# Performance work log

Hardware: AMD Instinct MI355X
Metric: run time of the kernel (lower is better)

Reference implementation:

```python
import math
import jax
import jax.numpy as jnp
import numpy as np
from jax import lax

HEADS = 4
TOPK = 8


def _gelu(x):
    return jax.nn.gelu(x, approximate=False)


def _ln(x, g, b, eps=1e-5):
    m = x.mean(-1, keepdims=True)
    v = ((x - m) ** 2).mean(-1, keepdims=True)
    return (x - m) * lax.rsqrt(v + eps) * g + b


def setup_inputs() -> dict:
    key = jax.random.key(0)
    ks = jax.random.split(key, 16)
    B, T, N, C, A = 16, 16, 196, 768, 192

    def w(k, shape, s=0.02):
        return jax.random.normal(k, shape, jnp.float32) * s

    return dict(
        x=w(ks[0], (B, T, N + 1, C), 1.0),
        down_w=w(ks[1], (A, C)), down_b=jnp.zeros((A,), jnp.float32),
        ldw_w=w(ks[2], (A, 1, 3, 3), 0.1),
        lpw_w=w(ks[3], (A, A), 0.05),
        lnorm_g=jnp.ones((A,), jnp.float32), lnorm_b=jnp.zeros((A,), jnp.float32),
        tdw_w=w(ks[4], (A, 1, 3), 0.1),
        tpw_w=w(ks[5], (A, A), 0.05),
        tmlp_w1=w(ks[6], (2 * A, A), 0.05), tmlp_b1=jnp.zeros((2 * A,), jnp.float32),
        tmlp_w2=w(ks[7], (A, 2 * A), 0.05), tmlp_b2=jnp.zeros((A,), jnp.float32),
        tnorm_g=jnp.ones((A,), jnp.float32), tnorm_b=jnp.zeros((A,), jnp.float32),
        attn_in_w=w(ks[8], (3 * A, A), 0.05), attn_in_b=jnp.zeros((3 * A,), jnp.float32),
        attn_out_w=w(ks[9], (A, A), 0.05), attn_out_b=jnp.zeros((A,), jnp.float32),
        aproj_w=w(ks[10], (A, A), 0.05), aproj_b=jnp.zeros((A,), jnp.float32),
        anorm_g=jnp.ones((A,), jnp.float32), anorm_b=jnp.zeros((A,), jnp.float32),
        gate_w1=w(ks[11], (A, 2 * A), 0.05), gate_b1=jnp.zeros((A,), jnp.float32),
        gate_w2=w(ks[12], (3 * A, A), 0.05), gate_b2=jnp.zeros((3 * A,), jnp.float32),
        up_w=w(ks[13], (C, A), 0.02), up_b=jnp.zeros((C,), jnp.float32),
        cls_w=w(ks[14], (C, A), 0.02), cls_b=jnp.zeros((C,), jnp.float32),
    )


def reference(x, down_w, down_b, ldw_w, lpw_w, lnorm_g, lnorm_b, tdw_w, tpw_w,
              tmlp_w1, tmlp_b1, tmlp_w2, tmlp_b2, tnorm_g, tnorm_b,
              attn_in_w, attn_in_b, attn_out_w, attn_out_b, aproj_w, aproj_b,
              anorm_g, anorm_b, gate_w1, gate_b1, gate_w2, gate_b2,
              up_w, up_b, cls_w, cls_b):
    cls_tok = x[:, :, :1, :]
    patch = x[:, :, 1:, :]
    b, t, n, _ = patch.shape
    hw = int(math.isqrt(n))
    a = down_w.shape[0]

    # down projection: [b,t,n,C] -> [b,t,n,A]
    ph = jnp.einsum('btnc,ac->btna', patch, down_w) + down_b
    # temporal difference, delta[:,0]=0
    delta = jnp.concatenate([jnp.zeros_like(ph[:, :1]), ph[:, 1:] - ph[:, :-1]], axis=1)

    # --- local path: depthwise 3x3 -> GELU -> pointwise 1x1 -> LN ---
    loc = ph.reshape(b * t, hw, hw, a).transpose(0, 3, 1, 2)  # (bt) a h w
    loc = lax.conv_general_dilated(loc, ldw_w, (1, 1), 'SAME',
                                   feature_group_count=a,
                                   dimension_numbers=('NCHW', 'OIHW', 'NCHW'))
    loc = _gelu(loc)
    loc = jnp.einsum('bchw,dc->bdhw', loc, lpw_w)
    loc = loc.transpose(0, 2, 3, 1).reshape(b, t, n, a)
    local = _ln(loc, lnorm_g, lnorm_b)

    # --- transition path: depthwise temporal conv -> GELU -> pointwise -> MLP -> LN ---
    tr = delta.transpose(0, 2, 3, 1).reshape(b * n, a, t)  # (bn) a t
    tr = lax.conv_general_dilated(tr, tdw_w, (1,), 'SAME',
                                  feature_group_count=a,
                                  dimension_numbers=('NCH', 'OIH', 'NCH'))
    tr = _gelu(tr)
    tr = jnp.einsum('nct,dc->ndt', tr, tpw_w)
    tr = tr.reshape(b, n, a, t).transpose(0, 3, 1, 2)  # b t n a
    h1 = _gelu(jnp.einsum('btna,ha->btnh', tr, tmlp_w1) + tmlp_b1)
    tr = jnp.einsum('btnh,ah->btna', h1, tmlp_w2) + tmlp_b2
    transition = _ln(tr, tnorm_g, tnorm_b)

    # --- relation anchor path: topk gather -> temporal MHA -> scatter_add -> LN ---
    kk = min(TOPK, n)
    sal = jnp.abs(delta).mean(-1)  # b t n
    _, idx = lax.top_k(sal, kk)    # b t k
    bi = jnp.arange(b)[:, None, None]
    ti = jnp.arange(t)[None, :, None]
    anchor = (ph + delta)[bi, ti, idx]  # b t k a
    tok = anchor.transpose(0, 2, 1, 3).reshape(b * kk, t, a)  # (bk) t a
    qkv = tok @ attn_in_w.T + attn_in_b
    q, k_, v = jnp.split(qkv, 3, axis=-1)
    dh = a // HEADS

    def heads(z):
        return z.reshape(b * kk, t, HEADS, dh).transpose(0, 2, 1, 3)

    q, k_, v = heads(q), heads(k_), heads(v)
    att = jax.nn.softmax(jnp.einsum('bhqd,bhkd->bhqk', q, k_) / math.sqrt(dh), axis=-1)
    out = jnp.einsum('bhqk,bhkd->bhqd', att, v).transpose(0, 2, 1, 3).reshape(b * kk, t, a)
    out = out @ attn_out_w.T + attn_out_b
    out = out @ aproj_w.T + aproj_b
    anchor_tok = out.reshape(b, kk, t, a).transpose(0, 2, 1, 3)  # b t k a
    anchor_map = jnp.zeros_like(ph).at[bi, ti, idx].add(anchor_tok)
    anchor_map = _ln(anchor_map, anorm_g, anorm_b)

    # --- softmax-gated 3-way fusion ---
    dp = jnp.abs(delta).mean((1, 2))      # b a
    ap = anchor_tok.mean((1, 2))          # b a
    g = jnp.concatenate([dp, ap], axis=-1)
    g = _gelu(g @ gate_w1.T + gate_b1) @ gate_w2.T + gate_b2
    gw = jax.nn.softmax(g.reshape(b, 3, a), axis=1)[:, :, None, None, :]
    fused = gw[:, 0] * local + gw[:, 1] * transition + gw[:, 2] * anchor_map

    patch_out = patch + fused @ up_w.T + up_b
    cls_out = cls_tok + fused.mean(2, keepdims=True) @ cls_w.T + cls_b
    return jnp.concatenate([cls_out, patch_out], axis=2)
```

## Files before the change

### kernel.cpp

```cpp
#include <hip/hip_runtime.h>
#include <hip/hip_bf16.h>
#include <math.h>

constexpr int Bb  = 16;
constexpr int Tt  = 16;
constexpr int Nn  = 196;
constexpr int Cc  = 768;
constexpr int Aa  = 192;
constexpr int KK  = 8;
constexpr int NCAND = 16;
constexpr int BT  = Bb * Tt;
constexpr int BTN = BT * Nn;
constexpr int BKT = Bb * KK * Tt;
constexpr size_t SZ = (size_t)BTN * Aa;

typedef unsigned short ushortt;
typedef __attribute__((ext_vector_type(8))) short bf16x8;
typedef __attribute__((ext_vector_type(4))) float f32x4;
typedef __attribute__((ext_vector_type(4))) unsigned short u16x4;
typedef __attribute__((ext_vector_type(8))) unsigned short u16x8;

static __device__ __forceinline__ float gelu_f(float x) {
  return 0.5f * x * (1.0f + erff(x * 0.7071067811865476f));
}
static __device__ __forceinline__ ushortt f2bf(float f) {
  __hip_bfloat16 h = __float2bfloat16(f);
  return *reinterpret_cast<ushortt*>(&h);
}
static __device__ __forceinline__ float bf2f(ushortt u) {
  return __uint_as_float(((unsigned)u) << 16);
}

template <typename AT, typename CT, int ROWMAP, int BIAS, int EPI>
__global__ __launch_bounds__(256) void gemm_mfma(
    const AT* __restrict__ Ain, const float* __restrict__ W,
    const float* __restrict__ bias, CT* __restrict__ Cout,
    const float* __restrict__ resid, int M, int Nc, int K) {
  constexpr int PIT = 72;
  __shared__ __align__(16) unsigned char smem[(2 * 64 * PIT + 2 * 96 * PIT) * 2];
  ushortt (*As)[64 * PIT] = (ushortt(*)[64 * PIT])smem;
  ushortt (*Bs)[96 * PIT] = (ushortt(*)[96 * PIT])(smem + 2 * 64 * PIT * 2);
  const int tid = threadIdx.x;

  const int ncb = gridDim.x;
  const int nwg = ncb * gridDim.y;
  const int bid = blockIdx.y * ncb + blockIdx.x;
  const int cpx = nwg >> 3;
  const int swz = (bid & 7) * cpx + (bid >> 3);
  const int row0 = (swz / ncb) * 64;
  const int col0 = (swz % ncb) * 96;

  const int wid = tid >> 6;
  const int lane = tid & 63;
  const int wr = wid >> 1;
  const int wc = wid & 1;
  const int l15 = lane & 15;
  const int kgrp = lane >> 4;

  const int q16 = tid & 15;
  const int q8 = tid & 7;

  const int nsteps = K >> 6;

  const float* arowf[4];
  const ushortt* arowb[2];
  if constexpr (sizeof(AT) == 4) {
#pragma unroll
    for (int p = 0; p < 4; ++p) {
      int r = row0 + (tid >> 4) + 16 * p;
      if (ROWMAP) {
        int bt = r / Nn;
        int n = r - bt * Nn;
        arowf[p] = (const float*)Ain + (size_t)(bt * (Nn + 1) + 1 + n) * K;
      } else {
        arowf[p] = (const float*)Ain + (size_t)r * K;
      }
    }
  } else {
#pragma unroll
    for (int p = 0; p < 2; ++p)
      arowb[p] = (const ushortt*)Ain + (size_t)(row0 + (tid >> 3) + 32 * p) * K;
  }
  const float* browp[6];
#pragma unroll
  for (int p = 0; p < 6; ++p)
    browp[p] = W + (size_t)(col0 + (tid >> 4) + 16 * p) * K;

  f32x4 acc[2][3];
#pragma unroll
  for (int i = 0; i < 2; ++i)
#pragma unroll
    for (int j = 0; j < 3; ++j) acc[i][j] = (f32x4){0.f, 0.f, 0.f, 0.f};

  float4 apre[4], bpre[6];
  u16x8 apreb[2];

#define STAGE_LOAD(k0)                                                       \
  if constexpr (sizeof(AT) == 4) {                                           \
    _Pragma("unroll") for (int p = 0; p < 4; ++p)                            \
        apre[p] = *(const float4*)(arowf[p] + (k0) + q16 * 4);               \
  } else {                                                                   \
    _Pragma("unroll") for (int p = 0; p < 2; ++p)                            \
        apreb[p] = *(const u16x8*)(arowb[p] + (k0) + q8 * 8);                \
  }                                                                          \
  _Pragma("unroll") for (int p = 0; p < 6; ++p)                              \
      bpre[p] = *(const float4*)(browp[p] + (k0) + q16 * 4);

#define STAGE_WRITE(buf)                                                     \
  if constexpr (sizeof(AT) == 4) {                                           \
    _Pragma("unroll") for (int p = 0; p < 4; ++p) {                          \
      u16x4 b = {f2bf(apre[p].x), f2bf(apre[p].y), f2bf(apre[p].z),          \
                 f2bf(apre[p].w)};                                           \
      *(u16x4*)&As[buf][((tid >> 4) + 16 * p) * PIT + q16 * 4] = b;          \
    }                                                                        \
  } else {                                                                   \
    _Pragma("unroll") for (int p = 0; p < 2; ++p)                            \
        *(u16x8*)&As[buf][((tid >> 3) + 32 * p) * PIT + q8 * 8] = apreb[p];  \
  }                                                                          \
  _Pragma("unroll") for (int p = 0; p < 6; ++p) {                            \
    u16x4 b = {f2bf(bpre[p].x), f2bf(bpre[p].y), f2bf(bpre[p].z),            \
               f2bf(bpre[p].w)};                                             \
    *(u16x4*)&Bs[buf][((tid >> 4) + 16 * p) * PIT + q16 * 4] = b;            \
  }

  STAGE_LOAD(0);
  STAGE_WRITE(0);
  __syncthreads();

  int cur = 0;
  for (int step = 0; step < nsteps; ++step) {
    const bool pref = (step + 1 < nsteps);
    if (pref) {
      int k0 = (step + 1) << 6;
      STAGE_LOAD(k0);
    }
#pragma unroll
    for (int kk = 0; kk < 2; ++kk) {
      bf16x8 af[2], bfv[3];
#pragma unroll
      for (int fm = 0; fm < 2; ++fm)
        af[fm] = *(const bf16x8*)&As[cur][(wr * 32 + fm * 16 + l15) * PIT +
                                          kk * 32 + kgrp * 8];
#pragma unroll
      for (int fn = 0; fn < 3; ++fn)
        bfv[fn] = *(const bf16x8*)&Bs[cur][(wc * 48 + fn * 16 + l15) * PIT +
                                           kk * 32 + kgrp * 8];
#pragma unroll
      for (int fm = 0; fm < 2; ++fm)
#pragma unroll
        for (int fn = 0; fn < 3; ++fn)
          acc[fm][fn] = __builtin_amdgcn_mfma_f32_16x16x32_bf16(
              af[fm], bfv[fn], acc[fm][fn], 0, 0, 0);
    }
    if (pref) {
      STAGE_WRITE(cur ^ 1);
    }
    __syncthreads();
    cur ^= 1;
  }
#undef STAGE_LOAD
#undef STAGE_WRITE

  constexpr int EP = 100;
  float* epi = (float*)smem;
#pragma unroll
  for (int fm = 0; fm < 2; ++fm) {
    int rl = wr * 32 + fm * 16 + kgrp * 4;
#pragma unroll
    for (int fn = 0; fn < 3; ++fn) {
      int cl = wc * 48 + fn * 16 + l15;
#pragma unroll
      for (int j = 0; j < 4; ++j)
        epi[(rl + j) * EP + cl] = acc[fm][fn][j];
    }
  }
  __syncthreads();
#pragma unroll
  for (int it = 0; it < 6; ++it) {
    int f = it * 256 + tid;
    int r = f / 24, c4 = f - r * 24;
    float4 v = *(const float4*)&epi[r * EP + c4 * 4];
    int c = col0 + c4 * 4;
    if (BIAS) {
      float4 bv = *(const float4*)(bias + c);
      v.x += bv.x; v.y += bv.y; v.z += bv.z; v.w += bv.w;
    }
    if (EPI == 1) {
      v.x = gelu_f(v.x); v.y = gelu_f(v.y);
      v.z = gelu_f(v.z); v.w = gelu_f(v.w);
    }
    int R = row0 + r;
    if constexpr (EPI == 2) {
      int bt2 = R / Nn, n2 = R - bt2 * Nn;
      size_t off = (size_t)(bt2 * (Nn + 1) + 1 + n2) * Nc + c;
      float4 rv = *(const float4*)(resid + off);
      v.x += rv.x; v.y += rv.y; v.z += rv.z; v.w += rv.w;
      *(float4*)((float*)Cout + off) = v;
    } else if constexpr (sizeof(CT) == 4) {
      *(float4*)((float*)Cout + (size_t)R * Nc + c) = v;
    } else {
      u16x4 ob = {f2bf(v.x), f2bf(v.y), f2bf(v.z), f2bf(v.w)};
      *(u16x4*)((ushortt*)Cout + (size_t)R * Nc + c) = ob;
    }
  }
}

__global__ void delta_kernel(const ushortt* __restrict__ ph,
                             ushortt* __restrict__ delta,
                             float* __restrict__ dppart) {
  int bt = blockIdx.x;
  int t = bt & 15;
  int a = threadIdx.x;
  const ushortt* cur = ph + (size_t)bt * Nn * Aa + a;
  ushortt* dl = delta + (size_t)bt * Nn * Aa + a;
  float acc = 0.f;
  if (t == 0) {
    for (int n = 0; n < Nn; ++n) dl[(size_t)n * Aa] = 0;
  } else {
    const ushortt* prev = cur - (size_t)Nn * Aa;
    for (int n = 0; n < Nn; ++n) {
      float d = bf2f(cur[(size_t)n * Aa]) - bf2f(prev[(size_t)n * Aa]);
      dl[(size_t)n * Aa] = f2bf(d);
      acc += fabsf(d);
    }
  }
  dppart[bt * Aa + a] = acc;
}

__global__ void sal_kernel(const ushortt* __restrict__ delta,
                           float* __restrict__ sal) {
  int row = blockIdx.x * 4 + (threadIdx.x >> 6);
  int lane = threadIdx.x & 63;
  const ushortt* d = delta + (size_t)row * Aa;
  float s = fabsf(bf2f(d[lane])) + fabsf(bf2f(d[lane + 64])) +
            fabsf(bf2f(d[lane + 128]));
#pragma unroll
  for (int off = 32; off > 0; off >>= 1) s += __shfl_xor(s, off, 64);
  if (lane == 0) sal[row] = s * (1.0f / 192.0f);
}

__global__ void topcand_kernel(const float* __restrict__ sal,
                               int* __restrict__ cand) {
  int bt = blockIdx.x;
  int lane = threadIdx.x;
  unsigned long long key[4];
#pragma unroll
  for (int j = 0; j < 4; ++j) {
    int n = lane + 64 * j;
    if (n < Nn) {
      unsigned fb = __float_as_uint(sal[(size_t)bt * Nn + n]);
      key[j] = ((unsigned long long)fb << 32) |
               (unsigned long long)(0xFFFFFFFFu - (unsigned)n);
    } else {
      key[j] = 0ULL;
    }
  }
  for (int r = 0; r < NCAND; ++r) {
    unsigned long long m = key[0];
    if (key[1] > m) m = key[1];
    if (key[2] > m) m = key[2];
    if (key[3] > m) m = key[3];
#pragma unroll
    for (int off = 32; off > 0; off >>= 1) {
      unsigned long long o = __shfl_xor(m, off, 64);
      if (o > m) m = o;
    }
    if (lane == 0)
      cand[bt * NCAND + r] = (int)(0xFFFFFFFFu - (unsigned)(m & 0xFFFFFFFFull));
#pragma unroll
    for (int j = 0; j < 4; ++j)
      if (key[j] == m) key[j] = 0ULL;
  }
}

__global__ void transpose_w(const float* __restrict__ w,
                            float* __restrict__ wT) {
  int e = blockIdx.x * 256 + threadIdx.x;
  int c = e / Aa, a = e - c * Aa;
  wT[e] = w[(size_t)a * Cc + c];
}

__global__ __launch_bounds__(192) void refine_kernel(
    const float* __restrict__ x, const float* __restrict__ wT,
    const int* __restrict__ cand, double* __restrict__ sal64) {
  int bt = blockIdx.x;
  int grp = blockIdx.y;
  int t = bt & 15;
  int a = threadIdx.x;
  if (t == 0) {
    if (a < 8) sal64[bt * NCAND + grp * 8 + a] = 0.0;
    return;
  }
  __shared__ double sdiff[8][Cc];
  const float* xt = x + ((size_t)bt * (Nn + 1) + 1) * Cc;
  const float* xp = xt - (size_t)(Nn + 1) * Cc;
  for (int g = 0; g < 8; ++g) {
    int n = cand[bt * NCAND + grp * 8 + g];
    const float* rt = xt + (size_t)n * Cc;
    const float* rp = xp + (size_t)n * Cc;
    for (int c = a; c < Cc; c += 192)
      sdiff[g][c] = (double)rt[c] - (double)rp[c];
  }
  __syncthreads();
  double acc[8] = {};
  for (int c = 0; c < Cc; ++c) {
    double wv = (double)wT[(size_t)c * Aa + a];
#pragma unroll
    for (int g = 0; g < 8; ++g) acc[g] = fma(wv, sdiff[g][c], acc[g]);
  }
  __shared__ double part[3][8];
  int wvx = a >> 6, ln = a & 63;
#pragma unroll
  for (int g = 0; g < 8; ++g) {
    double v = fabs(acc[g]);
#pragma unroll
    for (int off = 32; off > 0; off >>= 1) v += __shfl_xor(v, off, 64);
    if (ln == 0) part[wvx][g] = v;
  }
  __syncthreads();
  if (a < 8) {
    double s = part[0][a] + part[1][a] + part[2][a];
    sal64[bt * NCAND + grp * 8 + a] = s * (1.0 / 192.0);
  }
}

__global__ void select_kernel(const double* __restrict__ sal64,
                              const int* __restrict__ cand,
                              int* __restrict__ idx) {
  int bt = blockIdx.x;
  int t = bt & 15;
  int lane = threadIdx.x;
  if (t == 0) {
    if (lane < KK) idx[bt * KK + lane] = lane;
    return;
  }
  double v = (lane < NCAND) ? sal64[bt * NCAND + lane] : -1.0;
  int n = (lane < NCAND) ? cand[bt * NCAND + lane] : 0x7FFFFFFF;
  for (int r = 0; r < KK; ++r) {
    double bv = v;
    int bn = n, bl = lane;
#pragma unroll
    for (int off = 8; off >= 1; off >>= 1) {
      double ov = __shfl_xor(bv, off, 64);
      int on = __shfl_xor(bn, off, 64);
      int ol = __shfl_xor(bl, off, 64);
      if (ov > bv || (ov == bv && on < bn)) { bv = ov; bn = on; bl = ol; }
    }
    if (lane == 0) idx[bt * KK + r] = bn;
    if (lane == bl) v = -1.0;
  }
}

__global__ void gather_kernel(const ushortt* __restrict__ ph,
                              const ushortt* __restrict__ delta,
                              const int* __restrict__ idx,
                              ushortt* __restrict__ tok) {
  int row = blockIdx.x;
  int t = row & 15;
  int bk = row >> 4;
  int b = bk >> 3, k = bk & 7;
  int a = threadIdx.x;
  int n = idx[(b * 16 + t) * KK + k];
  size_t off = ((size_t)(b * 16 + t) * Nn + n) * Aa + a;
  tok[(size_t)row * Aa + a] = f2bf(bf2f(ph[off]) + bf2f(delta[off]));
}

__global__ __launch_bounds__(256) void attn_core(
    const float* __restrict__ qkv, float* __restrict__ o) {
  constexpr int P = 580;
  __shared__ float sq[16 * P];
  __shared__ float ssc[4][16][17];
  int bk = blockIdx.x;
  int tid = threadIdx.x;
  const float* src = qkv + (size_t)bk * 16 * 576;
  for (int e = tid; e < 16 * 144; e += 256) {
    int r = e / 144, c4 = e % 144;
    float4 v = *(const float4*)(src + r * 576 + c4 * 4);
    *(float4*)(&sq[r * P + c4 * 4]) = v;
  }
  __syncthreads();
  int h = tid >> 6, lane = tid & 63;
#pragma unroll
  for (int s4 = 0; s4 < 4; ++s4) {
    int e = lane + 64 * s4;
    int i = e >> 4, j = e & 15;
    const float* q = sq + i * P + h * 48;
    const float* k2 = sq + j * P + 192 + h * 48;
    float s = 0.f;
#pragma unroll
    for (int d = 0; d < 48; ++d) s = fmaf(q[d], k2[d], s);
    ssc[h][i][j] = s * 0.14433756729740643f;
  }
  __syncthreads();
  if (lane < 16) {
    float* r = ssc[h][lane];
    float mx = r[0];
    for (int j = 1; j < 16; ++j) mx = fmaxf(mx, r[j]);
    float sum = 0.f;
    for (int j = 0; j < 16; ++j) {
      float ev = expf(r[j] - mx);
      r[j] = ev;
      sum += ev;
    }
    float inv = 1.0f / sum;
    for (int j = 0; j < 16; ++j) r[j] *= inv;
  }
  __syncthreads();
#pragma unroll
  for (int s4 = 0; s4 < 12; ++s4) {
    int e = lane + 64 * s4;
    int i = e / 48, d = e - i * 48;
    float s = 0.f;
#pragma unroll
    for (int j = 0; j < 16; ++j)
      s = fmaf(ssc[h][i][j], sq[j * P + 384 + h * 48 + d], s);
    o[((size_t)bk * 16 + i) * 192 + h * 48 + d] = s;
  }
}

__global__ void appart_kernel(const float* __restrict__ attout,
                              float* __restrict__ appart) {
  int bk = blockIdx.x;
  int a = threadIdx.x;
  float s = 0.f;
  for (int t = 0; t < Tt; ++t)
    s += attout[((size_t)bk * Tt + t) * Aa + a];
  appart[bk * Aa + a] = s;
}

__global__ void ln32_kernel(float* __restrict__ buf,
                            const float* __restrict__ g,
                            const float* __restrict__ bb) {
  size_t row = (size_t)blockIdx.x * 4 + (threadIdx.x >> 6);
  int lane = threadIdx.x & 63;
  float* p = buf + row * Aa;
  float v0 = p[lane], v1 = p[lane + 64], v2 = p[lane + 128];
  float s = v0 + v1 + v2;
#pragma unroll
  for (int off = 32; off > 0; off >>= 1) s += __shfl_xor(s, off, 64);
  float m = s * (1.0f / 192.0f);
  float d0 = v0 - m, d1 = v1 - m, d2 = v2 - m;
  float ss = d0 * d0 + d1 * d1 + d2 * d2;
#pragma unroll
  for (int off = 32; off > 0; off >>= 1) ss += __shfl_xor(ss, off, 64);
  float inv = rsqrtf(ss * (1.0f / 192.0f) + 1e-5f);
  p[lane] = d0 * inv * g[lane] + bb[lane];
  p[lane + 64] = d1 * inv * g[lane + 64] + bb[lane + 64];
  p[lane + 128] = d2 * inv * g[lane + 128] + bb[lane + 128];
}

__global__ void conv2d_kernel(const ushortt* __restrict__ ph,
                              const float* __restrict__ ldw,
                              ushortt* __restrict__ og) {
  size_t e = (size_t)blockIdx.x * 256 + threadIdx.x;
  int a = (int)(e % Aa);
  size_t r = e / Aa;
  int n = (int)(r % Nn);
  int bt = (int)(r / Nn);
  int y = n / 14, x = n % 14;
  const ushortt* base = ph + (size_t)bt * Nn * Aa + a;
  const float* w = ldw + a * 9;
  float s = 0.f;
#pragma unroll
  for (int dy = -1; dy <= 1; ++dy) {
    int yy = y + dy;
    if (yy < 0 || yy >= 14) continue;
#pragma unroll
    for (int dx = -1; dx <= 1; ++dx) {
      int xc = x + dx;
      if (xc < 0 || xc >= 14) continue;
      s = fmaf(bf2f(base[(size_t)(yy * 14 + xc) * Aa]),
               w[(dy + 1) * 3 + (dx + 1)], s);
    }
  }
  og[e] = f2bf(gelu_f(s));
}

__global__ void conv1d_kernel(const ushortt* __restrict__ delta,
                              const float* __restrict__ tdw,
                              ushortt* __restrict__ og) {
  size_t e = (size_t)blockIdx.x * 256 + threadIdx.x;
  int a = (int)(e % Aa);
  size_t r = e / Aa;
  int n = (int)(r % Nn);
  int bt = (int)(r / Nn);
  int t = bt & 15, b = bt >> 4;
  const float* w = tdw + a * 3;
  float s = 0.f;
#pragma unroll
  for (int j = 0; j < 3; ++j) {
    int tt = t + j - 1;
    if (tt >= 0 && tt < Tt)
      s = fmaf(bf2f(delta[((size_t)(b * Tt + tt) * Nn + n) * Aa + a]), w[j], s);
  }
  og[e] = f2bf(gelu_f(s));
}

__global__ void ln_kernel(ushortt* __restrict__ buf,
                          const float* __restrict__ g,
                          const float* __restrict__ bb) {
  size_t row = (size_t)blockIdx.x * 4 + (threadIdx.x >> 6);
  int lane = threadIdx.x & 63;
  ushortt* p = buf + row * Aa;
  float v0 = bf2f(p[lane]), v1 = bf2f(p[lane + 64]), v2 = bf2f(p[lane + 128]);
  float s = v0 + v1 + v2;
#pragma unroll
  for (int off = 32; off > 0; off >>= 1) s += __shfl_xor(s, off, 64);
  float m = s * (1.0f / 192.0f);
  float d0 = v0 - m, d1 = v1 - m, d2 = v2 - m;
  float ss = d0 * d0 + d1 * d1 + d2 * d2;
#pragma unroll
  for (int off = 32; off > 0; off >>= 1) ss += __shfl_xor(ss, off, 64);
  float inv = rsqrtf(ss * (1.0f / 192.0f) + 1e-5f);
  p[lane] = f2bf(d0 * inv * g[lane] + bb[lane]);
  p[lane + 64] = f2bf(d1 * inv * g[lane + 64] + bb[lane + 64]);
  p[lane + 128] = f2bf(d2 * inv * g[lane + 128] + bb[lane + 128]);
}

__global__ void scatter_pos(const int* __restrict__ idx,
                            short* __restrict__ posmap) {
  int bt = blockIdx.x;
  int k = threadIdx.x;
  if (k < KK) posmap[bt * Nn + idx[bt * KK + k]] = (short)(k + 1);
}

__global__ void gate_kernel(const float* __restrict__ dppart,
                            const float* __restrict__ appart,
                            const float* __restrict__ w1,
                            const float* __restrict__ b1,
                            const float* __restrict__ w2,
                            const float* __restrict__ b2,
                            float* __restrict__ gw) {
  int b = blockIdx.x;
  __shared__ float sg[2 * Aa];
  __shared__ float sh[Aa];
  int tid = threadIdx.x;
  {
    float d = 0.f;
    for (int t2 = 0; t2 < Tt; ++t2) d += dppart[(b * Tt + t2) * Aa + tid];
    sg[tid] = d * (1.0f / 3136.0f);
    float a = 0.f;
    for (int k2 = 0; k2 < KK; ++k2) a += appart[(b * KK + k2) * Aa + tid];
    sg[Aa + tid] = a * (1.0f / 128.0f);
  }
  __syncthreads();
  {
    const float* w = w1 + (size_t)tid * 2 * Aa;
    float s = b1[tid];
#pragma unroll 8
    for (int j = 0; j < 2 * Aa; ++j) s = fmaf(sg[j], w[j], s);
    sh[tid] = gelu_f(s);
  }
  __syncthreads();
  float v[3];
#pragma unroll
  for (int i = 0; i < 3; ++i) {
    const float* w = w2 + (size_t)(i * Aa + tid) * Aa;
    float s = b2[i * Aa + tid];
#pragma unroll 8
    for (int j = 0; j < Aa; ++j) s = fmaf(sh[j], w[j], s);
    v[i] = s;
  }
  float mx = fmaxf(v[0], fmaxf(v[1], v[2]));
  float e0 = expf(v[0] - mx), e1 = expf(v[1] - mx), e2 = expf(v[2] - mx);
  float inv = 1.0f / (e0 + e1 + e2);
  gw[(b * 3 + 0) * Aa + tid] = e0 * inv;
  gw[(b * 3 + 1) * Aa + tid] = e1 * inv;
  gw[(b * 3 + 2) * Aa + tid] = e2 * inv;
}

__global__ void fused_kernel(const ushortt* __restrict__ local,
                             const ushortt* __restrict__ trans,
                             const float* __restrict__ attln,
                             const short* __restrict__ posmap,
                             const float* __restrict__ anb,
                             const float* __restrict__ gw,
                             ushortt* __restrict__ fused,
                             float* __restrict__ fmean) {
  int bt = blockIdx.x;
  int b = bt >> 4, t = bt & 15;
  int a = threadIdx.x;
  float g0 = gw[(b * 3 + 0) * Aa + a];
  float g1 = gw[(b * 3 + 1) * Aa + a];
  float g2 = gw[(b * 3 + 2) * Aa + a];
  float ab = anb[a];
  size_t base = (size_t)bt * Nn * Aa + a;
  float acc = 0.f;
  for (int n = 0; n < Nn; ++n) {
    size_t o = base + (size_t)n * Aa;
    short pos = posmap[bt * Nn + n];
    float am = pos ? attln[(((size_t)(b * KK + pos - 1) * Tt) + t) * Aa + a]
                   : ab;
    float f = g0 * bf2f(local[o]) + g1 * bf2f(trans[o]) + g2 * am;
    fused[o] = f2bf(f);
    acc += f;
  }
  fmean[bt * Aa + a] = acc;
}

__global__ void cls_kernel(const float* __restrict__ fmean,
                           const float* __restrict__ cw,
                           const float* __restrict__ cb,
                           const float* __restrict__ x,
                           float* __restrict__ out) {
  int bt = blockIdx.x;
  __shared__ float fm[Aa];
  int tid = threadIdx.x;
  if (tid < Aa) fm[tid] = fmean[bt * Aa + tid] * (1.0f / 196.0f);
  __syncthreads();
  for (int c = tid; c < Cc; c += 256) {
    const float* w = cw + (size_t)c * Aa;
    float s = cb[c];
#pragma unroll 8
    for (int a = 0; a < Aa; ++a) s = fmaf(fm[a], w[a], s);
    size_t off = (size_t)bt * (Nn + 1) * Cc + c;
    out[off] = x[off] + s;
  }
}

extern "C" void kernel_launch(void* const* d_in, const int* in_sizes, int n_in,
                              void* d_out, int out_size, void* d_ws,
                              size_t ws_size, hipStream_t stream) {
  const float* x = (const float*)d_in[0];
  const float* down_w = (const float*)d_in[1];
  const float* down_b = (const float*)d_in[2];
  const float* ldw_w = (const float*)d_in[3];
  const float* lpw_w = (const float*)d_in[4];
  const float* lnorm_g = (const float*)d_in[5];
  const float* lnorm_b = (const float*)d_in[6];
  const float* tdw_w = (const float*)d_in[7];
  const float* tpw_w = (const float*)d_in[8];
  const float* tmlp_w1 = (const float*)d_in[9];
  const float* tmlp_b1 = (const float*)d_in[10];
  const float* tmlp_w2 = (const float*)d_in[11];
  const float* tmlp_b2 = (const float*)d_in[12];
  const float* tnorm_g = (const float*)d_in[13];
  const float* tnorm_b = (const float*)d_in[14];
  const float* attn_in_w = (const float*)d_in[15];
  const float* attn_in_b = (const float*)d_in[16];
  const float* attn_out_w = (const float*)d_in[17];
  const float* attn_out_b = (const float*)d_in[18];
  const float* aproj_w = (const float*)d_in[19];
  const float* aproj_b = (const float*)d_in[20];
  const float* anorm_g = (const float*)d_in[21];
  const float* anorm_b = (const float*)d_in[22];
  const float* gate_w1 = (const float*)d_in[23];
  const float* gate_b1 = (const float*)d_in[24];
  const float* gate_w2 = (const float*)d_in[25];
  const float* gate_b2 = (const float*)d_in[26];
  const float* up_w = (const float*)d_in[27];
  const float* up_b = (const float*)d_in[28];
  const float* cls_w = (const float*)d_in[29];
  const float* cls_b = (const float*)d_in[30];
  float* out = (float*)d_out;

  float* ws = (float*)d_ws;
  float* W0 = ws;
  float* W1 = W0 + SZ;
  float* W2 = W1 + SZ;
  float* W3 = W2 + 2 * SZ;
  float* sal = W3 + SZ;
  float* attout = sal + BTN;
  float* dppart = attout + (size_t)BKT * Aa;
  float* appart = dppart + (size_t)BT * Aa;
  float* gw = appart + (size_t)Bb * KK * Aa;
  float* fmean = gw + (size_t)Bb * 3 * Aa;
  double* sal64 = (double*)(fmean + (size_t)BT * Aa);
  int* cand = (int*)(sal64 + (size_t)BT * NCAND);
  int* idx = cand + (size_t)BT * NCAND;
  float* wT = (float*)(idx + (size_t)BT * KK);
  short* posmap = (short*)(wT + (size_t)Cc * Aa);

  ushortt* ph_b    = (ushortt*)W0;
  ushortt* trp_b   = (ushortt*)W0;
  ushortt* delta_b = (ushortt*)W1;
  ushortt* trans_b = (ushortt*)W1;
  ushortt* locg_b  = (ushortt*)W2;
  ushortt* trg_b   = (ushortt*)W2;
  ushortt* h1_b    = (ushortt*)W2;
  ushortt* fused_b = (ushortt*)W2;
  ushortt* local_b = (ushortt*)W3;

  ushortt* tok_b = (ushortt*)W2;
  float* qkvb  = W2 + (size_t)BKT * Aa / 2;
  float* obuf  = qkvb + (size_t)BKT * 3 * Aa;
  float* proj1 = obuf + (size_t)BKT * Aa;

  gemm_mfma<float, ushortt, 1, 1, 0><<<dim3(2, 784), 256, 0, stream>>>(
      x, down_w, down_b, ph_b, nullptr, BTN, Aa, Cc);
  transpose_w<<<(Cc * Aa) / 256, 256, 0, stream>>>(down_w, wT);
  delta_kernel<<<BT, Aa, 0, stream>>>(ph_b, delta_b, dppart);
  sal_kernel<<<BTN / 4, 256, 0, stream>>>(delta_b, sal);
  topcand_kernel<<<BT, 64, 0, stream>>>(sal, cand);
  refine_kernel<<<dim3(BT, 2), 192, 0, stream>>>(x, wT, cand, sal64);
  select_kernel<<<BT, 64, 0, stream>>>(sal64, cand, idx);
  gather_kernel<<<BKT, Aa, 0, stream>>>(ph_b, delta_b, idx, tok_b);
  gemm_mfma<ushortt, float, 0, 1, 0><<<dim3(6, 32), 256, 0, stream>>>(
      tok_b, attn_in_w, attn_in_b, qkvb, nullptr, BKT, 3 * Aa, Aa);
  attn_core<<<Bb * KK, 256, 0, stream>>>(qkvb, obuf);
  gemm_mfma<float, float, 0, 1, 0><<<dim3(2, 32), 256, 0, stream>>>(
      obuf, attn_out_w, attn_out_b, proj1, nullptr, BKT, Aa, Aa);
  gemm_mfma<float, float, 0, 1, 0><<<dim3(2, 32), 256, 0, stream>>>(
      proj1, aproj_w, aproj_b, attout, nullptr, BKT, Aa, Aa);
  appart_kernel<<<Bb * KK, Aa, 0, stream>>>(attout, appart);
  ln32_kernel<<<BKT / 4, 256, 0, stream>>>(attout, anorm_g, anorm_b);
  hipMemsetAsync(posmap, 0, (size_t)BT * Nn * sizeof(short), stream);
  scatter_pos<<<BT, 64, 0, stream>>>(idx, posmap);
  conv2d_kernel<<<(unsigned)(SZ / 256), 256, 0, stream>>>(ph_b, ldw_w, locg_b);
  gemm_mfma<ushortt, ushortt, 0, 0, 0><<<dim3(2, 784), 256, 0, stream>>>(
      locg_b, lpw_w, nullptr, local_b, nullptr, BTN, Aa, Aa);
  ln_kernel<<<BTN / 4, 256, 0, stream>>>(local_b, lnorm_g, lnorm_b);
  conv1d_kernel<<<(unsigned)(SZ / 256), 256, 0, stream>>>(delta_b, tdw_w, trg_b);
  gemm_mfma<ushortt, ushortt, 0, 0, 0><<<dim3(2, 784), 256, 0, stream>>>(
      trg_b, tpw_w, nullptr, trp_b, nullptr, BTN, Aa, Aa);
  gemm_mfma<ushortt, ushortt, 0, 1, 1><<<dim3(4, 784), 256, 0, stream>>>(
      trp_b, tmlp_w1, tmlp_b1, h1_b, nullptr, BTN, 2 * Aa, Aa);
  gemm_mfma<ushortt, ushortt, 0, 1, 0><<<dim3(2, 784), 256, 0, stream>>>(
      h1_b, tmlp_w2, tmlp_b2, trans_b, nullptr, BTN, Aa, 2 * Aa);
  ln_kernel<<<BTN / 4, 256, 0, stream>>>(trans_b, tnorm_g, tnorm_b);
  gate_kernel<<<Bb, Aa, 0, stream>>>(dppart, appart, gate_w1, gate_b1,
                                     gate_w2, gate_b2, gw);
  fused_kernel<<<BT, Aa, 0, stream>>>(local_b, trans_b, attout, posmap,
                                      anorm_b, gw, fused_b, fmean);
  gemm_mfma<ushortt, float, 0, 1, 2><<<dim3(8, 784), 256, 0, stream>>>(
      fused_b, up_w, up_b, out, x, BTN, Cc, Aa);
  cls_kernel<<<BT, 256, 0, stream>>>(fmean, cls_w, cls_b, x, out);
}
```

Before: 608.3 us.

## Pre-convert weights to bf16 and use direct-to-LDS loads in bf16 GEMMs

Adds a kernel that converts all GEMM weights to bf16 once per call, plus a new GEMM variant. The variant loads bf16 A and B tiles straight into LDS with global_load_lds, using an XOR-swizzled layout and double buffering. Six bf16-input GEMMs now use it, which removes the per-tile fp32-to-bf16 weight conversion and the register staging of tile data. In exchange it launches an extra conversion kernel and needs more workspace, and it assumes 16-byte alignment and M, N and K that divide evenly into tiles.

Measured after the change: 579.7 us. 1.05x faster.

```diff
diff --git a/kernel.cpp b/kernel.cpp
--- a/kernel.cpp
+++ b/kernel.cpp
@@ -29,6 +29,180 @@
 }
 static __device__ __forceinline__ float bf2f(ushortt u) {
   return __uint_as_float(((unsigned)u) << 16);
+}
+static __device__ __forceinline__ void gload16(const void* g, void* l) {
+  __builtin_amdgcn_global_load_lds(
+      (const __attribute__((address_space(1))) void*)g,
+      (__attribute__((address_space(3))) void*)l, 16, 0, 0);
+}
+
+constexpr int S_down   = Aa * Cc;
+constexpr int S_attnin = 3 * Aa * Aa;
+constexpr int S_sq     = Aa * Aa;
+constexpr int S_t      = 2 * Aa * Aa;
+constexpr int O1 = S_down;
+constexpr int O2 = O1 + S_attnin;
+constexpr int O3 = O2 + S_sq;
+constexpr int O4 = O3 + S_sq;
+constexpr int O5 = O4 + S_sq;
+constexpr int O6 = O5 + S_sq;
+constexpr int O7 = O6 + S_t;
+constexpr int O8 = O7 + S_t;
+constexpr int OTOT = O8 + S_down;
+
+__global__ void cvtw_kernel(const float* __restrict__ w0,
+                            const float* __restrict__ w1,
+                            const float* __restrict__ w2,
+                            const float* __restrict__ w3,
+                            const float* __restrict__ w4,
+                            const float* __restrict__ w5,
+                            const float* __restrict__ w6,
+                            const float* __restrict__ w7,
+                            const float* __restrict__ w8,
+                            ushortt* __restrict__ outw) {
+  int e = blockIdx.x * 256 + threadIdx.x;
+  const float* src;
+  int off;
+  if (e < O1)      { src = w0; off = 0;  }
+  else if (e < O2) { src = w1; off = O1; }
+  else if (e < O3) { src = w2; off = O2; }
+  else if (e < O4) { src = w3; off = O3; }
+  else if (e < O5) { src = w4; off = O4; }
+  else if (e < O6) { src = w5; off = O5; }
+  else if (e < O7) { src = w6; off = O6; }
+  else if (e < O8) { src = w7; off = O7; }
+  else             { src = w8; off = O8; }
+  outw[e] = f2bf(src[e - off]);
+}
+
+template <typename CT, int BIAS, int EPI>
+__global__ __launch_bounds__(256) void gemm_lds(
+    const ushortt* __restrict__ Ain, const ushortt* __restrict__ Wb,
+    const float* __restrict__ bias, CT* __restrict__ Cout,
+    const float* __restrict__ resid, int M, int Nc, int K) {
+  __shared__ __align__(16) unsigned char smem[40960];
+  ushortt (*As)[64 * 64] = (ushortt(*)[64 * 64])smem;
+  ushortt (*Bs)[96 * 64] = (ushortt(*)[96 * 64])(smem + 2 * 64 * 64 * 2);
+  const int tid = threadIdx.x;
+
+  const int ncb = gridDim.x;
+  const int nwg = ncb * gridDim.y;
+  const int bid = blockIdx.y * ncb + blockIdx.x;
+  const int cpx = nwg >> 3;
+  const int swz = (bid & 7) * cpx + (bid >> 3);
+  const int row0 = (swz / ncb) * 64;
+  const int col0 = (swz % ncb) * 96;
+
+  const int wid = tid >> 6;
+  const int lane = tid & 63;
+  const int wr = wid >> 1;
+  const int wc = wid & 1;
+  const int l15 = lane & 15;
+  const int kgrp = lane >> 4;
+
+  const int lr = lane >> 3;
+  const int lc = 8 * ((lane & 7) ^ lr);
+
+  f32x4 acc[2][3];
+#pragma unroll
+  for (int i = 0; i < 2; ++i)
+#pragma unroll
+    for (int j = 0; j < 3; ++j) acc[i][j] = (f32x4){0.f, 0.f, 0.f, 0.f};
+
+#define ISSUE(buf, k0)                                                       \
+  do {                                                                       \
+    _Pragma("unroll") for (int i = 0; i < 2; ++i) {                          \
+      int j = 2 * wid + i;                                                   \
+      const ushortt* g =                                                     \
+          Ain + (size_t)(row0 + 8 * j + lr) * K + (k0) + lc;                 \
+      gload16(g, &As[buf][j * 512]);                                         \
+    }                                                                        \
+    _Pragma("unroll") for (int i = 0; i < 3; ++i) {                          \
+      int j = 3 * wid + i;                                                   \
+      const ushortt* g =                                                     \
+          Wb + (size_t)(col0 + 8 * j + lr) * K + (k0) + lc;                  \
+      gload16(g, &Bs[buf][j * 512]);                                         \
+    }                                                                        \
+  } while (0)
+
+  ISSUE(0, 0);
+  __syncthreads();
+
+  const int nsteps = K >> 6;
+  int cur = 0;
+  for (int step = 0; step < nsteps; ++step) {
+    const bool pref = (step + 1 < nsteps);
+    if (pref) ISSUE(cur ^ 1, (step + 1) << 6);
+#pragma unroll
+    for (int kk = 0; kk < 2; ++kk) {
+      const int cb = kk * 64 + kgrp * 16;
+      bf16x8 af[2], bfv[3];
+#pragma unroll
+      for (int fm = 0; fm < 2; ++fm) {
+        int r = wr * 32 + fm * 16 + l15;
+        af[fm] = *(const bf16x8*)&As[cur][r * 64 +
+                                          ((cb ^ ((r & 7) << 4)) >> 1)];
+      }
+#pragma unroll
+      for (int fn = 0; fn < 3; ++fn) {
+        int r = wc * 48 + fn * 16 + l15;
+        bfv[fn] = *(const bf16x8*)&Bs[cur][r * 64 +
+                                           ((cb ^ ((r & 7) << 4)) >> 1)];
+      }
+#pragma unroll
+      for (int fm = 0; fm < 2; ++fm)
+#pragma unroll
+        for (int fn = 0; fn < 3; ++fn)
+          acc[fm][fn] = __builtin_amdgcn_mfma_f32_16x16x32_bf16(
+              af[fm], bfv[fn], acc[fm][fn], 0, 0, 0);
+    }
+    __syncthreads();
+    cur ^= 1;
+  }
+#undef ISSUE
+
+  constexpr int EP = 100;
+  float* epi = (float*)smem;
+#pragma unroll
+  for (int fm = 0; fm < 2; ++fm) {
+    int rl = wr * 32 + fm * 16 + kgrp * 4;
+#pragma unroll
+    for (int fn = 0; fn < 3; ++fn) {
+      int cl = wc * 48 + fn * 16 + l15;
+#pragma unroll
+      for (int j = 0; j < 4; ++j)
+        epi[(rl + j) * EP + cl] = acc[fm][fn][j];
+    }
+  }
+  __syncthreads();
+#pragma unroll
+  for (int it = 0; it < 6; ++it) {
+    int f = it * 256 + tid;
+    int r = f / 24, c4 = f - r * 24;
+    float4 v = *(const float4*)&epi[r * EP + c4 * 4];
+    int c = col0 + c4 * 4;
+    if (BIAS) {
+      float4 bv = *(const float4*)(bias + c);
+      v.x += bv.x; v.y += bv.y; v.z += bv.z; v.w += bv.w;
+    }
+    if (EPI == 1) {
+      v.x = gelu_f(v.x); v.y = gelu_f(v.y);
+      v.z = gelu_f(v.z); v.w = gelu_f(v.w);
+    }
+    int R = row0 + r;
+    if constexpr (EPI == 2) {
+      int bt2 = R / Nn, n2 = R - bt2 * Nn;
+      size_t off = (size_t)(bt2 * (Nn + 1) + 1 + n2) * Nc + c;
+      float4 rv = *(const float4*)(resid + off);
+      v.x += rv.x; v.y += rv.y; v.z += rv.z; v.w += rv.w;
+      *(float4*)((float*)Cout + off) = v;
+    } else if constexpr (sizeof(CT) == 4) {
+      *(float4*)((float*)Cout + (size_t)R * Nc + c) = v;
+    } else {
+      u16x4 ob = {f2bf(v.x), f2bf(v.y), f2bf(v.z), f2bf(v.w)};
+      *(u16x4*)((ushortt*)Cout + (size_t)R * Nc + c) = ob;
+    }
+  }
 }
 
 template <typename AT, typename CT, int ROWMAP, int BIAS, int EPI>
@@ -670,6 +844,14 @@
   int* idx = cand + (size_t)BT * NCAND;
   float* wT = (float*)(idx + (size_t)BT * KK);
   short* posmap = (short*)(wT + (size_t)Cc * Aa);
+  ushortt* wbuf = (ushortt*)(posmap + (size_t)BT * Nn);
+
+  ushortt* wb_attnin = wbuf + O1;
+  ushortt* wb_lpw    = wbuf + O4;
+  ushortt* wb_tpw    = wbuf + O5;
+  ushortt* wb_t1     = wbuf + O6;
+  ushortt* wb_t2     = wbuf + O7;
+  ushortt* wb_up     = wbuf + O8;
 
   ushortt* ph_b    = (ushortt*)W0;
   ushortt* trp_b   = (ushortt*)W0;
@@ -686,17 +868,20 @@
   float* obuf  = qkvb + (size_t)BKT * 3 * Aa;
   float* proj1 = obuf + (size_t)BKT * Aa;
 
+  cvtw_kernel<<<OTOT / 256, 256, 0, stream>>>(
+      down_w, attn_in_w, attn_out_w, aproj_w, lpw_w, tpw_w, tmlp_w1,
+      tmlp_w2, up_w, wbuf);
+  transpose_w<<<(Cc * Aa) / 256, 256, 0, stream>>>(down_w, wT);
   gemm_mfma<float, ushortt, 1, 1, 0><<<dim3(2, 784), 256, 0, stream>>>(
       x, down_w, down_b, ph_b, nullptr, BTN, Aa, Cc);
-  transpose_w<<<(Cc * Aa) / 256, 256, 0, stream>>>(down_w, wT);
   delta_kernel<<<BT, Aa, 0, stream>>>(ph_b, delta_b, dppart);
   sal_kernel<<<BTN / 4, 256, 0, stream>>>(delta_b, sal);
   topcand_kernel<<<BT, 64, 0, stream>>>(sal, cand);
   refine_kernel<<<dim3(BT, 2), 192, 0, stream>>>(x, wT, cand, sal64);
   select_kernel<<<BT, 64, 0, stream>>>(sal64, cand, idx);
   gather_kernel<<<BKT, Aa, 0, stream>>>(ph_b, delta_b, idx, tok_b);
-  gemm_mfma<ushortt, float, 0, 1, 0><<<dim3(6, 32), 256, 0, stream>>>(
-      tok_b, attn_in_w, attn_in_b, qkvb, nullptr, BKT, 3 * Aa, Aa);
+  gemm_lds<float, 1, 0><<<dim3(6, 32), 256, 0, stream>>>(
+      tok_b, wb_attnin, attn_in_b, qkvb, nullptr, BKT, 3 * Aa, Aa);
   attn_core<<<Bb * KK, 256, 0, stream>>>(qkvb, obuf);
   gemm_mfma<float, float, 0, 1, 0><<<dim3(2, 32), 256, 0, stream>>>(
       obuf, attn_out_w, attn_out_b, proj1, nullptr, BKT, Aa, Aa);
@@ -707,22 +892,22 @@
   hipMemsetAsync(posmap, 0, (size_t)BT * Nn * sizeof(short), stream);
   scatter_pos<<<BT, 64, 0, stream>>>(idx, posmap);
   conv2d_kernel<<<(unsigned)(SZ / 256), 256, 0, stream>>>(ph_b, ldw_w, locg_b);
-  gemm_mfma<ushortt, ushortt, 0, 0, 0><<<dim3(2, 784), 256, 0, stream>>>(
-      locg_b, lpw_w, nullptr, local_b, nullptr, BTN, Aa, Aa);
+  gemm_lds<ushortt, 0, 0><<<dim3(2, 784), 256, 0, stream>>>(
+      locg_b, wb_lpw, nullptr, local_b, nullptr, BTN, Aa, Aa);
   ln_kernel<<<BTN / 4, 256, 0, stream>>>(local_b, lnorm_g, lnorm_b);
   conv1d_kernel<<<(unsigned)(SZ / 256), 256, 0, stream>>>(delta_b, tdw_w, trg_b);
-  gemm_mfma<ushortt, ushortt, 0, 0, 0><<<dim3(2, 784), 256, 0, stream>>>(
-      trg_b, tpw_w, nullptr, trp_b, nullptr, BTN, Aa, Aa);
-  gemm_mfma<ushortt, ushortt, 0, 1, 1><<<dim3(4, 784), 256, 0, stream>>>(
-      trp_b, tmlp_w1, tmlp_b1, h1_b, nullptr, BTN, 2 * Aa, Aa);
-  gemm_mfma<ushortt, ushortt, 0, 1, 0><<<dim3(2, 784), 256, 0, stream>>>(
-      h1_b, tmlp_w2, tmlp_b2, trans_b, nullptr, BTN, Aa, 2 * Aa);
+  gemm_lds<ushortt, 0, 0><<<dim3(2, 784), 256, 0, stream>>>(
+      trg_b, wb_tpw, nullptr, trp_b, nullptr, BTN, Aa, Aa);
+  gemm_lds<ushortt, 1, 1><<<dim3(4, 784), 256, 0, stream>>>(
+      trp_b, wb_t1, tmlp_b1, h1_b, nullptr, BTN, 2 * Aa, Aa);
+  gemm_lds<ushortt, 1, 0><<<dim3(2, 784), 256, 0, stream>>>(
+      h1_b, wb_t2, tmlp_b2, trans_b, nullptr, BTN, Aa, 2 * Aa);
   ln_kernel<<<BTN / 4, 256, 0, stream>>>(trans_b, tnorm_g, tnorm_b);
   gate_kernel<<<Bb, Aa, 0, stream>>>(dppart, appart, gate_w1, gate_b1,
                                      gate_w2, gate_b2, gw);
   fused_kernel<<<BT, Aa, 0, stream>>>(local_b, trans_b, attout, posmap,
                                       anorm_b, gw, fused_b, fmean);
-  gemm_mfma<ushortt, float, 0, 1, 2><<<dim3(8, 784), 256, 0, stream>>>(
-      fused_b, up_w, up_b, out, x, BTN, Cc, Aa);
+  gemm_lds<float, 1, 2><<<dim3(8, 784), 256, 0, stream>>>(
+      fused_b, wb_up, up_b, out, x, BTN, Cc, Aa);
   cls_kernel<<<BT, 256, 0, stream>>>(fmean, cls_w, cls_b, x, out);
 }
```
